# Kernel optimization log

Hardware: AMD Instinct MI355X
Metric: run time of the kernel (lower is better)

The kernel has to match this reference:

```python
import jax, jax.numpy as jnp
import numpy as np

B, CIN, N = 4, 128, 4096
CKEY, COUT = 64, 128

def setup_inputs() -> dict:
    key = jax.random.key(0)
    k1, k2, k3, k4 = jax.random.split(key, 4)
    x = jax.random.normal(k1, (B, CIN, N), dtype=jnp.float32)
    # Conv1d(kernel_size=1, bias=False) weights as [out, in] matrices
    Wq = jax.random.normal(k2, (CKEY, CIN), dtype=jnp.float32) * (1.0 / np.sqrt(CIN))
    Wk = jax.random.normal(k3, (CKEY, CIN), dtype=jnp.float32) * (1.0 / np.sqrt(CIN))
    Wv = jax.random.normal(k4, (COUT, CIN), dtype=jnp.float32) * (1.0 / np.sqrt(CIN))
    return {"x": x, "Wq": Wq, "Wk": Wk, "Wv": Wv}

def reference(x, Wq, Wk, Wv):
    # 1x1 conv projections: [B, C, N] -> [B, C', N]
    Q = jnp.einsum('ki,bin->bkn', Wq, x)   # [B, CKEY, N]
    K = jnp.einsum('ki,bin->bkn', Wk, x)   # [B, CKEY, N]
    V = jnp.einsum('oi,bin->bon', Wv, x)   # [B, COUT, N]
    # A = softmax(Q^T K) over last dim -- NOTE: no 1/sqrt(d) scaling, as in original
    scores = jnp.einsum('bkn,bkm->bnm', Q, K)     # [B, N, N]
    A = jax.nn.softmax(scores, axis=2)
    # out = (A @ V^T)^T -> [B, COUT, N]
    out = jnp.einsum('bnm,bom->bon', A, V)
    return out
```

## Files before the change

kernel.cpp:

```cpp
#include <hip/hip_runtime.h>
#include <hip/hip_bf16.h>

#define NN    4096
#define BB    4
#define CIN_  128
#define COUT_ 128

typedef __attribute__((ext_vector_type(8))) short bf16x8;
typedef __attribute__((ext_vector_type(4))) short bf16x4;
typedef __attribute__((ext_vector_type(4))) float f32x4;
typedef __attribute__((ext_vector_type(2))) int   i32x2;

#define MFMA16 __builtin_amdgcn_mfma_f32_16x16x32_bf16
#define SWK(row, g) ((((row) << 6)) + ((((g) ^ ((row) & 7))) << 3))

__device__ __forceinline__ float bf2f(short s) {
    union { unsigned int u; float f; } c; c.u = ((unsigned int)(unsigned short)s) << 16; return c.f;
}
__device__ __forceinline__ short f2bf(float f) {
    union { float f; unsigned int u; } c; c.f = f;
    unsigned int r = c.u + 0x7fffu + ((c.u >> 16) & 1u);
    return (short)(r >> 16);
}
__device__ __forceinline__ float fexp2(float x) {
#if __has_builtin(__builtin_amdgcn_exp2f)
    return __builtin_amdgcn_exp2f(x);
#else
    return exp2f(x);
#endif
}
__device__ __forceinline__ unsigned int pack_bf16(float a, float b) {
    union { float f; unsigned int u; } ca, cb; ca.f = a; cb.f = b;
    unsigned int ua = ca.u + 0x8000u, ub = cb.u + 0x8000u;
#if __has_builtin(__builtin_amdgcn_perm)
    return __builtin_amdgcn_perm(ub, ua, 0x07060302u);
#else
    return (ua >> 16) | (ub & 0xffff0000u);
#endif
}

__global__ __launch_bounds__(256) void proj_kernel(const float* __restrict__ x,
                                                   const float* __restrict__ Wq,
                                                   const float* __restrict__ Wk,
                                                   const float* __restrict__ Wv,
                                                   short* __restrict__ Qh, short* __restrict__ Ql,
                                                   short* __restrict__ Kh, short* __restrict__ Kl,
                                                   short* __restrict__ Vb) {
    __shared__ __align__(16) short xsh[16 * 64 * 8];
    __shared__ __align__(16) short xsl[16 * 64 * 8];

    int tid  = threadIdx.x;
    int b    = blockIdx.y;
    int gz   = blockIdx.z;
    int gn0  = blockIdx.x * 64;
    int wave = tid >> 6;
    int lane = tid & 63;
    int quad = lane >> 4;
    int l15  = lane & 15;

    const float* xb = x + (size_t)b * CIN_ * NN + gn0;
#pragma unroll
    for (int rep = 0; rep < 4; ++rep) {
        int slot = rep * 256 + tid;
        int c = slot >> 6, n = slot & 63;
        bf16x8 h8, l8;
#pragma unroll
        for (int j = 0; j < 8; ++j) {
            float f = xb[(c * 8 + j) * NN + n];
            short h = f2bf(f);
            h8[j] = h;
            l8[j] = f2bf(f - bf2f(h));
        }
        *(bf16x8*)(xsh + (c * 64 + n) * 8) = h8;
        *(bf16x8*)(xsl + (c * 64 + n) * 8) = l8;
    }
    __syncthreads();

    int rg = gz * 4 + wave;

    const float* wrow;
    float scale = 1.0f;
    if (rg < 4)      { wrow = Wq + (rg * 16 + l15) * CIN_; scale = 1.4426950408889634f; }
    else if (rg < 8) { wrow = Wk + ((rg - 4) * 16 + l15) * CIN_; }
    else             { wrow = Wv + ((rg - 8) * 16 + l15) * CIN_; }

    bf16x8 wh[4], wl[4];
#pragma unroll
    for (int kc = 0; kc < 4; ++kc) {
        const float* wp = wrow + kc * 32 + quad * 8;
#pragma unroll
        for (int j = 0; j < 8; ++j) {
            float w = wp[j] * scale;
            short h = f2bf(w);
            wh[kc][j] = h;
            wl[kc][j] = f2bf(w - bf2f(h));
        }
    }

    f32x4 acc[4];
#pragma unroll
    for (int ct = 0; ct < 4; ++ct) acc[ct] = (f32x4){0.f, 0.f, 0.f, 0.f};

#pragma unroll
    for (int kc = 0; kc < 4; ++kc) {
#pragma unroll
        for (int ct = 0; ct < 4; ++ct) {
            bf16x8 xh = *(const bf16x8*)(xsh + (((kc * 4 + quad) * 64) + ct * 16 + l15) * 8);
            bf16x8 xl = *(const bf16x8*)(xsl + (((kc * 4 + quad) * 64) + ct * 16 + l15) * 8);
            acc[ct] = MFMA16(wh[kc], xh, acc[ct], 0, 0, 0);
            acc[ct] = MFMA16(wh[kc], xl, acc[ct], 0, 0, 0);
            acc[ct] = MFMA16(wl[kc], xh, acc[ct], 0, 0, 0);
        }
    }

    if (rg < 8) {
        short* H = (rg < 4) ? Qh : Kh;
        short* L = (rg < 4) ? Ql : Kl;
        int rb    = (rg < 4) ? rg : (rg - 4);
        int chunk = rb * 2 + (quad >> 1);
        int sub   = (quad & 1) * 4;
#pragma unroll
        for (int ct = 0; ct < 4; ++ct) {
            int n = gn0 + ct * 16 + l15;
            bf16x4 h4, l4;
#pragma unroll
            for (int r = 0; r < 4; ++r) {
                float f = acc[ct][r];
                short h = f2bf(f);
                h4[r] = h;
                l4[r] = f2bf(f - bf2f(h));
            }
            *(bf16x4*)(H + (((b * 8 + chunk) * NN) + n) * 8 + sub) = h4;
            *(bf16x4*)(L + (((b * 8 + chunk) * NN) + n) * 8 + sub) = l4;
        }
    } else {
        int o0 = rg * 16 + quad * 4 - 128;
#pragma unroll
        for (int ct = 0; ct < 4; ++ct) {
            int n = gn0 + ct * 16 + l15;
#pragma unroll
            for (int r = 0; r < 4; ++r)
                Vb[((size_t)(b * COUT_ + o0 + r)) * NN + n] = f2bf(acc[ct][r]);
        }
    }
}

__global__ __launch_bounds__(256, 2) void flash_kernel(const short* __restrict__ Qh,
                                                       const short* __restrict__ Ql,
                                                       const short* __restrict__ Kh,
                                                       const short* __restrict__ Kl,
                                                       const short* __restrict__ Vb,
                                                       float* __restrict__ outp,
                                                       float* __restrict__ lsum,
                                                       int S, int direct) {
    __shared__ __align__(16) short VT[128 * 64];
    __shared__ __align__(16) short PW[4 * 32 * 64];

    int tid  = threadIdx.x;
    int bx   = blockIdx.x;
    int b    = bx / S;
    int s    = bx - b * S;
    int qt   = blockIdx.y;
    int wave = tid >> 6;
    int lane = tid & 63;
    int quad = lane >> 4;
    int l15  = lane & 15;

    int nq0 = qt * 128 + wave * 32 + l15;
    bf16x8 qh0[2], qh1[2], ql0[2], ql1[2];
#pragma unroll
    for (int u = 0; u < 2; ++u) {
        int nq = nq0 + u * 16;
        qh0[u] = *(const bf16x8*)(Qh + (((b * 8 + quad)     * NN) + nq) * 8);
        qh1[u] = *(const bf16x8*)(Qh + (((b * 8 + 4 + quad) * NN) + nq) * 8);
        ql0[u] = *(const bf16x8*)(Ql + (((b * 8 + quad)     * NN) + nq) * 8);
        ql1[u] = *(const bf16x8*)(Ql + (((b * 8 + 4 + quad) * NN) + nq) * 8);
    }

    f32x4 O[2][8];
#pragma unroll
    for (int u = 0; u < 2; ++u)
#pragma unroll
        for (int f = 0; f < 8; ++f) O[u][f] = (f32x4){0.f, 0.f, 0.f, 0.f};
    float lp[2] = {0.f, 0.f};

    int vrow = tid & 127, vc0 = (tid >> 7) * 4;
    short* pwb = PW + wave * 2048;

    int KPS   = NN / S;
    int kb    = s * KPS;
    int iters = KPS / 64;

    const short* KhB = Kh + (size_t)b * 8 * NN * 8;
    const short* KlB = Kl + (size_t)b * 8 * NN * 8;
    const short* VbB = Vb + (size_t)b * COUT_ * NN;

    bf16x8 nv[4];
#pragma unroll
    for (int q = 0; q < 4; ++q)
        nv[q] = *(const bf16x8*)(VbB + (size_t)vrow * NN + kb + (vc0 + q) * 8);

    for (int it = 0; it < iters; ++it) {
        bf16x8 kh0[4], kh1[4], kl0[4], kl1[4];
#pragma unroll
        for (int f = 0; f < 4; ++f) {
            int row = kb + f * 16 + l15;
            kh0[f] = *(const bf16x8*)(KhB + ((quad       * NN) + row) * 8);
            kh1[f] = *(const bf16x8*)(KhB + (((4 + quad) * NN) + row) * 8);
            kl0[f] = *(const bf16x8*)(KlB + ((quad       * NN) + row) * 8);
            kl1[f] = *(const bf16x8*)(KlB + (((4 + quad) * NN) + row) * 8);
        }

#pragma unroll
        for (int q = 0; q < 4; ++q)
            *(bf16x8*)(VT + SWK(vrow, vc0 + q)) = nv[q];
        __syncthreads();

        if (it + 1 < iters) {
            int nb = kb + 64;
#pragma unroll
            for (int q = 0; q < 4; ++q)
                nv[q] = *(const bf16x8*)(VbB + (size_t)vrow * NN + nb + (vc0 + q) * 8);
        }

        f32x4 sA[2][4];
#pragma unroll
        for (int f = 0; f < 4; ++f) {
#pragma unroll
            for (int u = 0; u < 2; ++u) {
                f32x4 acc = (f32x4){0.f, 0.f, 0.f, 0.f};
                acc = MFMA16(kh0[f], qh0[u], acc, 0, 0, 0);
                acc = MFMA16(kh1[f], qh1[u], acc, 0, 0, 0);
                acc = MFMA16(kl0[f], qh0[u], acc, 0, 0, 0);
                acc = MFMA16(kl1[f], qh1[u], acc, 0, 0, 0);
                acc = MFMA16(kh0[f], ql0[u], acc, 0, 0, 0);
                acc = MFMA16(kh1[f], ql1[u], acc, 0, 0, 0);
                sA[u][f] = acc;
            }
        }

#pragma unroll
        for (int u = 0; u < 2; ++u) {
            int row = u * 16 + l15;
#pragma unroll
            for (int f = 0; f < 4; ++f) {
                float p0 = fexp2(sA[u][f][0]);
                float p1 = fexp2(sA[u][f][1]);
                float p2 = fexp2(sA[u][f][2]);
                float p3 = fexp2(sA[u][f][3]);
                lp[u] += (p0 + p1) + (p2 + p3);
                unsigned int w0 = pack_bf16(p0, p1);
                unsigned int w1 = pack_bf16(p2, p3);
                *(i32x2*)(pwb + SWK(row, f * 2 + (quad >> 1)) + (quad & 1) * 4) =
                    (i32x2){(int)w0, (int)w1};
            }
        }

#pragma unroll
        for (int g = 0; g < 2; ++g) {
            bf16x8 pb0 = *(const bf16x8*)(pwb + SWK(l15,      g * 4 + quad));
            bf16x8 pb1 = *(const bf16x8*)(pwb + SWK(16 + l15, g * 4 + quad));
#pragma unroll
            for (int f8 = 0; f8 < 8; ++f8) {
                bf16x8 vA = *(const bf16x8*)(VT + SWK(f8 * 16 + l15, g * 4 + quad));
                O[0][f8] = MFMA16(vA, pb0, O[0][f8], 0, 0, 0);
                O[1][f8] = MFMA16(vA, pb1, O[1][f8], 0, 0, 0);
            }
        }
        __syncthreads();
        kb += 64;
    }

#pragma unroll
    for (int u = 0; u < 2; ++u) {
        lp[u] += __shfl_xor(lp[u], 16, 64);
        lp[u] += __shfl_xor(lp[u], 32, 64);
    }

#pragma unroll
    for (int u = 0; u < 2; ++u) {
        int n = nq0 + u * 16;
        if (direct) {
            float inv = 1.f / lp[u];
#pragma unroll
            for (int f8 = 0; f8 < 8; ++f8)
#pragma unroll
                for (int r = 0; r < 4; ++r) {
                    int o = f8 * 16 + quad * 4 + r;
                    outp[((size_t)(b * COUT_ + o)) * NN + n] = O[u][f8][r] * inv;
                }
        } else {
#pragma unroll
            for (int f8 = 0; f8 < 8; ++f8)
#pragma unroll
                for (int r = 0; r < 4; ++r) {
                    int o = f8 * 16 + quad * 4 + r;
                    outp[((size_t)((b * S + s) * COUT_ + o)) * NN + n] = O[u][f8][r];
                }
            if (quad == 0) lsum[(b * S + s) * NN + n] = lp[u];
        }
    }
}

__global__ __launch_bounds__(256, 4) void merge_kernel(const float* __restrict__ Opart,
                                                       const float* __restrict__ lsum,
                                                       float* __restrict__ out, int S) {
    int idx = blockIdx.x * 256 + threadIdx.x;
    int n0  = (idx & (NN / 4 - 1)) * 4;
    int rest = idx >> 10;
    int o = rest & (COUT_ - 1);
    int b = rest >> 7;

    f32x4 den = (f32x4){0.f, 0.f, 0.f, 0.f};
    f32x4 acc = (f32x4){0.f, 0.f, 0.f, 0.f};
    for (int s = 0; s < S; ++s) {
        f32x4 l  = *(const f32x4*)(lsum + (b * S + s) * NN + n0);
        f32x4 ov = *(const f32x4*)(Opart + ((size_t)((b * S + s) * COUT_ + o)) * NN + n0);
#pragma unroll
        for (int j = 0; j < 4; ++j) {
            den[j] += l[j];
            acc[j] += ov[j];
        }
    }
    f32x4 res;
#pragma unroll
    for (int j = 0; j < 4; ++j) res[j] = acc[j] / den[j];
    *(f32x4*)(out + ((size_t)(b * COUT_ + o)) * NN + n0) = res;
}

extern "C" void kernel_launch(void* const* d_in, const int* in_sizes, int n_in,
                              void* d_out, int out_size, void* d_ws, size_t ws_size,
                              hipStream_t stream) {
    const float* x  = (const float*)d_in[0];
    const float* Wq = (const float*)d_in[1];
    const float* Wk = (const float*)d_in[2];
    const float* Wv = (const float*)d_in[3];

    char* ws = (char*)d_ws;
    short* Qh = (short*)ws;
    short* Ql = Qh + 1048576;
    short* Kh = Ql + 1048576;
    short* Kl = Kh + 1048576;
    short* Vb = Kl + 1048576;
    size_t base = 4ull * 2097152 + 4194304;
    const size_t MLSZ  = (size_t)BB * NN * 4;
    const size_t OPART = 8388608;

    int S;
    if      (ws_size >= base + 4 * (MLSZ + OPART)) S = 4;
    else if (ws_size >= base + 2 * (MLSZ + OPART)) S = 2;
    else                                           S = 1;
    int direct = (S == 1);

    float* lsum  = (float*)(ws + base);
    float* Opart = (float*)(ws + base + (size_t)S * MLSZ);

    proj_kernel<<<dim3(NN / 64, BB, 4), 256, 0, stream>>>(x, Wq, Wk, Wv, Qh, Ql, Kh, Kl, Vb);
    flash_kernel<<<dim3(BB * S, NN / 128), 256, 0, stream>>>(
        Qh, Ql, Kh, Kl, Vb, direct ? (float*)d_out : Opart, lsum, S, direct);
    if (!direct)
        merge_kernel<<<BB * COUT_ * NN / 4 / 256, 256, 0, stream>>>(Opart, lsum, (float*)d_out, S);
}
```

Measured before the change: 124.0 us.

## Double-buffer V tile in LDS and prefetch next K fragments in registers

The flash attention loop now ping-pongs between two LDS buffers for the V tile and unrolls by two, so the trailing __syncthreads per iteration is removed. K fragments for the next tile are loaded into a second register set while the current tile's score MFMAs and softmax run, hiding global-load latency. The cost is double the VT shared memory and another 64 bf16x8 registers per thread, which may spill or lower occupancy under launch_bounds(256,2).

```diff
diff --git a/kernel.cpp b/kernel.cpp
--- a/kernel.cpp
+++ b/kernel.cpp
@@ -153,7 +153,7 @@
                                                        float* __restrict__ outp,
                                                        float* __restrict__ lsum,
                                                        int S, int direct) {
-    __shared__ __align__(16) short VT[128 * 64];
+    __shared__ __align__(16) short VT[2][128 * 64];
     __shared__ __align__(16) short PW[4 * 32 * 64];
 
     int tid  = threadIdx.x;
@@ -188,7 +188,7 @@
     short* pwb = PW + wave * 2048;
 
     int KPS   = NN / S;
-    int kb    = s * KPS;
+    int kbase = s * KPS;
     int iters = KPS / 64;
 
     const short* KhB = Kh + (size_t)b * 8 * NN * 8;
@@ -196,80 +196,99 @@
     const short* VbB = Vb + (size_t)b * COUT_ * NN;
 
     bf16x8 nv[4];
-#pragma unroll
-    for (int q = 0; q < 4; ++q)
-        nv[q] = *(const bf16x8*)(VbB + (size_t)vrow * NN + kb + (vc0 + q) * 8);
-
-    for (int it = 0; it < iters; ++it) {
-        bf16x8 kh0[4], kh1[4], kl0[4], kl1[4];
-#pragma unroll
-        for (int f = 0; f < 4; ++f) {
-            int row = kb + f * 16 + l15;
-            kh0[f] = *(const bf16x8*)(KhB + ((quad       * NN) + row) * 8);
-            kh1[f] = *(const bf16x8*)(KhB + (((4 + quad) * NN) + row) * 8);
-            kl0[f] = *(const bf16x8*)(KlB + ((quad       * NN) + row) * 8);
-            kl1[f] = *(const bf16x8*)(KlB + (((4 + quad) * NN) + row) * 8);
-        }
-
-#pragma unroll
-        for (int q = 0; q < 4; ++q)
-            *(bf16x8*)(VT + SWK(vrow, vc0 + q)) = nv[q];
+    bf16x8 kAh0[4], kAh1[4], kAl0[4], kAl1[4];
+    bf16x8 kBh0[4], kBh1[4], kBl0[4], kBl1[4];
+
+#define LOAD_K(set, kb_)                                                        \
+    _Pragma("unroll")                                                           \
+    for (int f = 0; f < 4; ++f) {                                               \
+        int row = (kb_) + f * 16 + l15;                                         \
+        set##h0[f] = *(const bf16x8*)(KhB + ((quad       * NN) + row) * 8);     \
+        set##h1[f] = *(const bf16x8*)(KhB + (((4 + quad) * NN) + row) * 8);     \
+        set##l0[f] = *(const bf16x8*)(KlB + ((quad       * NN) + row) * 8);     \
+        set##l1[f] = *(const bf16x8*)(KlB + (((4 + quad) * NN) + row) * 8);     \
+    }
+
+#define LOAD_V(kb_)                                                             \
+    _Pragma("unroll")                                                           \
+    for (int q = 0; q < 4; ++q)                                                 \
+        nv[q] = *(const bf16x8*)(VbB + (size_t)vrow * NN + (kb_) + (vc0 + q) * 8);
+
+#define COMMIT_V(p)                                                             \
+    _Pragma("unroll")                                                           \
+    for (int q = 0; q < 4; ++q)                                                 \
+        *(bf16x8*)(VT[p] + SWK(vrow, vc0 + q)) = nv[q];
+
+#define PHASE_COMPUTE(set, p, kb_, more)                                        \
+    {                                                                           \
+        f32x4 sA[2][4];                                                         \
+        _Pragma("unroll")                                                       \
+        for (int f = 0; f < 4; ++f) {                                           \
+            _Pragma("unroll")                                                   \
+            for (int u = 0; u < 2; ++u) {                                       \
+                f32x4 acc = (f32x4){0.f, 0.f, 0.f, 0.f};                        \
+                acc = MFMA16(set##h0[f], qh0[u], acc, 0, 0, 0);                 \
+                acc = MFMA16(set##h1[f], qh1[u], acc, 0, 0, 0);                 \
+                acc = MFMA16(set##l0[f], qh0[u], acc, 0, 0, 0);                 \
+                acc = MFMA16(set##l1[f], qh1[u], acc, 0, 0, 0);                 \
+                acc = MFMA16(set##h0[f], ql0[u], acc, 0, 0, 0);                 \
+                acc = MFMA16(set##h1[f], ql1[u], acc, 0, 0, 0);                 \
+                sA[u][f] = acc;                                                 \
+            }                                                                   \
+        }                                                                       \
+        more                                                                    \
+        _Pragma("unroll")                                                       \
+        for (int u = 0; u < 2; ++u) {                                           \
+            int row = u * 16 + l15;                                             \
+            _Pragma("unroll")                                                   \
+            for (int f = 0; f < 4; ++f) {                                       \
+                float p0 = fexp2(sA[u][f][0]);                                  \
+                float p1 = fexp2(sA[u][f][1]);                                  \
+                float p2 = fexp2(sA[u][f][2]);                                  \
+                float p3 = fexp2(sA[u][f][3]);                                  \
+                lp[u] += (p0 + p1) + (p2 + p3);                                 \
+                unsigned int w0 = pack_bf16(p0, p1);                            \
+                unsigned int w1 = pack_bf16(p2, p3);                            \
+                *(i32x2*)(pwb + SWK(row, f * 2 + (quad >> 1)) + (quad & 1) * 4) \
+                    = (i32x2){(int)w0, (int)w1};                                \
+            }                                                                   \
+        }                                                                       \
+        _Pragma("unroll")                                                       \
+        for (int g = 0; g < 2; ++g) {                                           \
+            bf16x8 pb0 = *(const bf16x8*)(pwb + SWK(l15,      g * 4 + quad));   \
+            bf16x8 pb1 = *(const bf16x8*)(pwb + SWK(16 + l15, g * 4 + quad));   \
+            _Pragma("unroll")                                                   \
+            for (int f8 = 0; f8 < 8; ++f8) {                                    \
+                bf16x8 vA = *(const bf16x8*)(VT[p] + SWK(f8 * 16 + l15, g * 4 + quad)); \
+                O[0][f8] = MFMA16(vA, pb0, O[0][f8], 0, 0, 0);                  \
+                O[1][f8] = MFMA16(vA, pb1, O[1][f8], 0, 0, 0);                  \
+            }                                                                   \
+        }                                                                       \
+    }
+
+    LOAD_V(kbase);
+    LOAD_K(kA, kbase);
+
+    for (int it = 0; it < iters; it += 2) {
+        int kb0 = kbase + it * 64;
+        COMMIT_V(0);
         __syncthreads();
-
+        if (it + 1 < iters) { LOAD_V(kb0 + 64); }
+        PHASE_COMPUTE(kA, 0, kb0,
+                      if (it + 1 < iters) { LOAD_K(kB, kb0 + 64); })
         if (it + 1 < iters) {
-            int nb = kb + 64;
-#pragma unroll
-            for (int q = 0; q < 4; ++q)
-                nv[q] = *(const bf16x8*)(VbB + (size_t)vrow * NN + nb + (vc0 + q) * 8);
-        }
-
-        f32x4 sA[2][4];
-#pragma unroll
-        for (int f = 0; f < 4; ++f) {
-#pragma unroll
-            for (int u = 0; u < 2; ++u) {
-                f32x4 acc = (f32x4){0.f, 0.f, 0.f, 0.f};
-                acc = MFMA16(kh0[f], qh0[u], acc, 0, 0, 0);
-                acc = MFMA16(kh1[f], qh1[u], acc, 0, 0, 0);
-                acc = MFMA16(kl0[f], qh0[u], acc, 0, 0, 0);
-                acc = MFMA16(kl1[f], qh1[u], acc, 0, 0, 0);
-                acc = MFMA16(kh0[f], ql0[u], acc, 0, 0, 0);
-                acc = MFMA16(kh1[f], ql1[u], acc, 0, 0, 0);
-                sA[u][f] = acc;
-            }
-        }
-
-#pragma unroll
-        for (int u = 0; u < 2; ++u) {
-            int row = u * 16 + l15;
-#pragma unroll
-            for (int f = 0; f < 4; ++f) {
-                float p0 = fexp2(sA[u][f][0]);
-                float p1 = fexp2(sA[u][f][1]);
-                float p2 = fexp2(sA[u][f][2]);
-                float p3 = fexp2(sA[u][f][3]);
-                lp[u] += (p0 + p1) + (p2 + p3);
-                unsigned int w0 = pack_bf16(p0, p1);
-                unsigned int w1 = pack_bf16(p2, p3);
-                *(i32x2*)(pwb + SWK(row, f * 2 + (quad >> 1)) + (quad & 1) * 4) =
-                    (i32x2){(int)w0, (int)w1};
-            }
-        }
-
-#pragma unroll
-        for (int g = 0; g < 2; ++g) {
-            bf16x8 pb0 = *(const bf16x8*)(pwb + SWK(l15,      g * 4 + quad));
-            bf16x8 pb1 = *(const bf16x8*)(pwb + SWK(16 + l15, g * 4 + quad));
-#pragma unroll
-            for (int f8 = 0; f8 < 8; ++f8) {
-                bf16x8 vA = *(const bf16x8*)(VT + SWK(f8 * 16 + l15, g * 4 + quad));
-                O[0][f8] = MFMA16(vA, pb0, O[0][f8], 0, 0, 0);
-                O[1][f8] = MFMA16(vA, pb1, O[1][f8], 0, 0, 0);
-            }
-        }
-        __syncthreads();
-        kb += 64;
-    }
+            COMMIT_V(1);
+            __syncthreads();
+            if (it + 2 < iters) { LOAD_V(kb0 + 128); }
+            PHASE_COMPUTE(kB, 1, kb0 + 64,
+                          if (it + 2 < iters) { LOAD_K(kA, kb0 + 128); })
+        }
+    }
+
+#undef LOAD_K
+#undef LOAD_V
+#undef COMMIT_V
+#undef PHASE_COMPUTE
 
 #pragma unroll
     for (int u = 0; u < 2; ++u) {
```

New measurement: 171.5 us. +38.3%, slower.
